# Performance work log

Hardware: AMD Instinct MI355X
Metric: run time of the kernel (lower is better)

Reference implementation:

```python
import jax, jax.numpy as jnp
import numpy as np

B, T, F, E, H = 8, 64, 16, 256, 8


def setup_inputs() -> dict:
    key = jax.random.key(0)
    ks = jax.random.split(key, 12)
    s = 1.0 / np.sqrt(E)
    return {
        "query": jax.random.normal(ks[0], (B, T, F, E), dtype=jnp.float32),
        "key": jax.random.normal(ks[1], (B, T, F, E), dtype=jnp.float32),
        "value": jax.random.normal(ks[2], (B, T, F, E), dtype=jnp.float32),
        "Wq": jax.random.uniform(ks[3], (E, E), jnp.float32, -s, s),
        "bq": jax.random.uniform(ks[4], (E,), jnp.float32, -s, s),
        "Wk": jax.random.uniform(ks[5], (E, E), jnp.float32, -s, s),
        "bk": jax.random.uniform(ks[6], (E,), jnp.float32, -s, s),
        "Wv": jax.random.uniform(ks[7], (E, E), jnp.float32, -s, s),
        "bv": jax.random.uniform(ks[8], (E,), jnp.float32, -s, s),
        "Wo": jax.random.uniform(ks[9], (E, E), jnp.float32, -s, s),
        "bo": jax.random.uniform(ks[10], (E,), jnp.float32, -s, s),
        "num_heads": H,
    }


def reference(query, key, value, Wq, bq, Wk, bk, Wv, bv, Wo, bo, num_heads):
    b, t, f, e = query.shape
    h = num_heads
    d = e // h

    def split_heads(x):
        # (b,t,f,e) -> (b,h,t,f,d)
        return x.reshape(b, t, f, h, d).transpose(0, 3, 1, 2, 4)

    q = split_heads(query @ Wq + bq)
    k = split_heads(key @ Wk + bk)
    v = split_heads(value @ Wv + bv)

    # scores[b,h,t,f,x,y] = k[b,h,t,f]·q[b,h,x,y] / sqrt(d)
    scores = jnp.einsum('bhtfd,bhxyd->bhtfxy', k, q) / jnp.sqrt(jnp.asarray(d, q.dtype))
    # Softmax2d on (b*h, t*f, t, f): softmax over channel = key positions (t*f)
    scores = scores.reshape(b, h, t * f, t, f)
    w = jax.nn.softmax(scores, axis=2)
    # out einsum 'bhtfxy,bhtfd->bhtfd': value scaled by total weight over queries
    s = w.sum(axis=(3, 4)).reshape(b, h, t, f)  # (b,h,t,f)
    out = v * s[..., None]
    out = out.transpose(0, 2, 3, 1, 4).reshape(b, t, f, e)
    return out @ Wo + bo
```

## Files before the change

### kernel.cpp

```cpp
#include <hip/hip_runtime.h>
#include <hip/hip_bf16.h>
#include <cstdint>
#include <cstddef>

constexpr int E = 256;
constexpr int H = 8;
constexpr int D = 32;
constexpr int N = 1024;
constexpr int R = 8192;
constexpr int BH = 64;
constexpr float SCALE = 0.17677669529663687f;
constexpr float LOG2E = 1.4426950408889634f;
constexpr float QSCALE = SCALE * LOG2E;


typedef __attribute__((ext_vector_type(8))) short short8;
typedef __attribute__((ext_vector_type(4))) short short4v;
typedef __attribute__((ext_vector_type(4))) float f32x4;

static __device__ __forceinline__ short bf16bits(float x) {
    __hip_bfloat16 h = __float2bfloat16(x);
    return *reinterpret_cast<short*>(&h);
}
static __device__ __forceinline__ float bf16tof(short s) {
    unsigned int u = ((unsigned int)(unsigned short)s) << 16;
    return *reinterpret_cast<float*>(&u);
}

__global__ __launch_bounds__(256) void convw_kernel(
    const float* __restrict__ Wq, const float* __restrict__ Wk,
    const float* __restrict__ Wv, const float* __restrict__ Wo,
    short* __restrict__ Wt4f)
{
    const int w = blockIdx.y;
    const float* src = (w == 0) ? Wq : (w == 1) ? Wk : (w == 2) ? Wv : Wo;
    const int tr = blockIdx.x >> 2, tc = blockIdx.x & 3;
    __shared__ float tile[64][65];
    const int tid = threadIdx.x;
    #pragma unroll
    for (int it = 0; it < 16; ++it) {
        int idx = tid + it * 256;
        int r = idx >> 6, c = idx & 63;
        tile[r][c] = src[(size_t)(tr * 64 + r) * E + tc * 64 + c];
    }
    __syncthreads();
    #pragma unroll
    for (int it = 0; it < 16; ++it) {
        int idx = tid + it * 256;
        int kk = idx >> 6, nn = idx & 63;
        int k = tr * 64 + kk, n = tc * 64 + nn;
        size_t didx = ((((size_t)w * 16 + (n >> 4)) * 32 + (k >> 3)) * 16 + (n & 15)) * 8 + (k & 7);
        Wt4f[didx] = bf16bits(tile[kk][nn]);
    }
}

__global__ __launch_bounds__(256) void proj_mfma(
    const float* __restrict__ q_in, const float* __restrict__ k_in, const float* __restrict__ v_in,
    const short* __restrict__ Wt4f,
    const float* __restrict__ bq, const float* __restrict__ bk, const float* __restrict__ bv,
    short* __restrict__ Qf, short* __restrict__ Kf,
    short* __restrict__ Vf, float* __restrict__ sfull)
{
    const int gid   = blockIdx.x;
    const int low3  = gid & 7;
    const int nhalf = (gid >> 3) & 1;
    const int p     = (gid >> 4) * 8 + low3;
    const int which = p >> 7;
    const int mblk  = p & 127;

    const float* X  = (which == 0) ? q_in : (which == 1) ? k_in : v_in;
    const float* bias = (which == 0) ? bq : (which == 1) ? bk : bv;

    if (which == 2) {
        int zb = mblk * 2 + nhalf;
        sfull[(size_t)zb * 256 + threadIdx.x] = 0.f;
    }

    const int wave = threadIdx.x >> 6, lane = threadIdx.x & 63;
    const int l15 = lane & 15, lhi = lane >> 4;
    const int m0 = mblk * 64 + wave * 16;
    const int n0 = nhalf * 128;

    __shared__ short Dt[4][16][16];

    const float* xrow = X + (size_t)(m0 + l15) * E + lhi * 8;

    f32x4 acc[8] = {};
    for (int k0 = 0; k0 < E; k0 += 32) {
        float4 a0 = *(const float4*)(xrow + k0);
        float4 a1 = *(const float4*)(xrow + k0 + 4);
        short at[8];
        at[0] = bf16bits(a0.x); at[1] = bf16bits(a0.y);
        at[2] = bf16bits(a0.z); at[3] = bf16bits(a0.w);
        at[4] = bf16bits(a1.x); at[5] = bf16bits(a1.y);
        at[6] = bf16bits(a1.z); at[7] = bf16bits(a1.w);
        short8 af = *(short8*)at;
        #pragma unroll
        for (int nt = 0; nt < 8; ++nt) {
            size_t bidx = ((((size_t)which * 16 + (n0 >> 4) + nt) * 32 + (k0 >> 3) + lhi) * 16 + l15) * 8;
            short8 bf = *(const short8*)(Wt4f + bidx);
            acc[nt] = __builtin_amdgcn_mfma_f32_16x16x32_bf16(af, bf, acc[nt], 0, 0, 0);
        }
    }

    short* dst;
    const int L = lane;
    #pragma unroll
    for (int nt = 0; nt < 8; ++nt) {
        const int ncol = n0 + nt * 16;
        #pragma unroll
        for (int j = 0; j < 4; ++j) {
            float v = acc[nt][j] + bias[ncol + l15];
            short sv = (which == 0) ? bf16bits(v * QSCALE) : bf16bits(v);
            Dt[wave][lhi * 4 + j][l15] = sv;
        }
        short4v rv = *(const short4v*)&Dt[wave][(L >> 1) & 15][(L >> 5) * 8 + (L & 1) * 4];

        size_t off;
        if (which == 2) {
            int tile = m0 >> 4;
            int kc0  = ncol >> 3;
            off = ((size_t)tile * 32 + kc0) * 128;
            dst = Vf;
        } else {
            int b = m0 >> 10, nl0 = m0 & (N - 1);
            int h = ncol >> 5, dd0 = ncol & 31;
            int tile = (b * H + h) * 64 + (nl0 >> 4);
            off = ((size_t)tile * 4 + (dd0 >> 3)) * 128;
            dst = (which == 0) ? Qf : Kf;
        }
        *(short4v*)(dst + off + (size_t)L * 4) = rv;
    }
}

__global__ __launch_bounds__(512, 4) void scores_fused(
    const short* __restrict__ Qf, const short* __restrict__ Kf,
    float* __restrict__ sfull)
{
    const int bh = blockIdx.x;
    const int mc = blockIdx.y;
    const int tid  = threadIdx.x;
    const int wave = tid >> 6;
    const int lane = tid & 63;
    const int l15  = lane & 15;
    const int lhi  = lane >> 4;

    const short* Qb = Qf + (size_t)bh * 32768;
    const short* Kb = Kf + (size_t)bh * 32768;

    __shared__ float zred[8][16];
    __shared__ float cinvS[16];

    short8 qf = *(const short8*)(Qb + ((size_t)mc * 4 + lhi) * 128 + l15 * 8);

    float z[4] = {0.f, 0.f, 0.f, 0.f};
    short4v ep[8];

    #pragma unroll
    for (int ntl = 0; ntl < 8; ++ntl) {
        int nt = wave * 8 + ntl;
        short8 kf = *(const short8*)(Kb + ((size_t)nt * 4 + lhi) * 128 + l15 * 8);
        f32x4 acc = {0.f, 0.f, 0.f, 0.f};
        acc = __builtin_amdgcn_mfma_f32_16x16x32_bf16(qf, kf, acc, 0, 0, 0);
        float e0 = exp2f(acc[0]), e1 = exp2f(acc[1]);
        float e2 = exp2f(acc[2]), e3 = exp2f(acc[3]);
        z[0] += e0; z[1] += e1; z[2] += e2; z[3] += e3;
        short4v pk = { bf16bits(e0), bf16bits(e1), bf16bits(e2), bf16bits(e3) };
        ep[ntl] = pk;
    }

    #pragma unroll
    for (int j = 0; j < 4; ++j) {
        float v = z[j];
        v += __shfl_xor(v, 1); v += __shfl_xor(v, 2);
        v += __shfl_xor(v, 4); v += __shfl_xor(v, 8);
        z[j] = v;
    }
    if (l15 == 0) {
        #pragma unroll
        for (int j = 0; j < 4; ++j)
            zred[wave][lhi * 4 + j] = z[j];
    }
    __syncthreads();
    if (tid < 16) {
        float zs = 0.f;
        #pragma unroll
        for (int w = 0; w < 8; ++w) zs += zred[w][tid];
        cinvS[tid] = 1.0f / zs;
    }
    __syncthreads();

    float ci[4];
    #pragma unroll
    for (int j = 0; j < 4; ++j) ci[j] = cinvS[lhi * 4 + j];

    float* sf = sfull + (size_t)bh * N;
    #pragma unroll
    for (int ntl = 0; ntl < 8; ++ntl) {
        int nt = wave * 8 + ntl;
        float rp = bf16tof(ep[ntl][0]) * ci[0] + bf16tof(ep[ntl][1]) * ci[1]
                 + bf16tof(ep[ntl][2]) * ci[2] + bf16tof(ep[ntl][3]) * ci[3];
        rp += __shfl_xor(rp, 16);
        rp += __shfl_xor(rp, 32);
        if (lane < 16) atomicAdd(&sf[nt * 16 + l15], rp);
    }
}

__global__ __launch_bounds__(256) void out_mfma(
    const short* __restrict__ Vf, const float* __restrict__ sfull,
    const short* __restrict__ Wt4f,
    const float* __restrict__ bo, float* __restrict__ out)
{
    const int gid  = blockIdx.x;
    const int low3 = gid & 7;
    const int nb   = (gid >> 3) & 3;
    const int q    = (gid >> 5) * 8 + low3;

    const int wave = threadIdx.x >> 6, lane = threadIdx.x & 63;
    const int l15 = lane & 15, lhi = lane >> 4;
    const int m0 = q * 64 + wave * 16;
    const int n0 = nb * 64;

    const int r = m0 + l15;
    const int b = r >> 10, nl = r & (N - 1);
    float sarr[8];
    #pragma unroll
    for (int h = 0; h < 8; ++h)
        sarr[h] = sfull[(size_t)(b * H + h) * N + nl];

    const short* vt = Vf + (size_t)(m0 >> 4) * 4096;

    f32x4 acc[4] = {};
    for (int k0 = 0; k0 < E; k0 += 32) {
        const float s = sarr[k0 >> 5];
        short8 vv = *(const short8*)(vt + ((size_t)(k0 >> 3) + lhi) * 128 + l15 * 8);
        short at[8];
        #pragma unroll
        for (int i = 0; i < 8; ++i) at[i] = bf16bits(bf16tof(vv[i]) * s);
        short8 af = *(short8*)at;
        #pragma unroll
        for (int nt = 0; nt < 4; ++nt) {
            size_t bidx = ((((size_t)3 * 16 + (n0 >> 4) + nt) * 32 + (k0 >> 3) + lhi) * 16 + l15) * 8;
            short8 bf = *(const short8*)(Wt4f + bidx);
            acc[nt] = __builtin_amdgcn_mfma_f32_16x16x32_bf16(af, bf, acc[nt], 0, 0, 0);
        }
    }
    #pragma unroll
    for (int nt = 0; nt < 4; ++nt) {
        #pragma unroll
        for (int j = 0; j < 4; ++j) {
            int m = m0 + lhi * 4 + j;
            int n = n0 + nt * 16 + l15;
            out[(size_t)m * E + n] = acc[nt][j] + bo[n];
        }
    }
}

extern "C" void kernel_launch(void* const* d_in, const int* in_sizes, int n_in,
                              void* d_out, int out_size, void* d_ws, size_t ws_size,
                              hipStream_t stream) {
    const float* q_in = (const float*)d_in[0];
    const float* k_in = (const float*)d_in[1];
    const float* v_in = (const float*)d_in[2];
    const float* Wq = (const float*)d_in[3];
    const float* bq = (const float*)d_in[4];
    const float* Wk = (const float*)d_in[5];
    const float* bk = (const float*)d_in[6];
    const float* Wv = (const float*)d_in[7];
    const float* bv = (const float*)d_in[8];
    const float* Wo = (const float*)d_in[9];
    const float* bo = (const float*)d_in[10];
    float* out = (float*)d_out;

    char* ws = (char*)d_ws;
    short* Wt4f  = (short*)ws;
    short* Qf    = (short*)(ws + (512u << 10));
    short* Kf    = (short*)(ws + (4u << 20) + (512u << 10));
    short* Vf    = (short*)(ws + (8u << 20) + (512u << 10));
    float* sfull = (float*)(ws + (12u << 20) + (512u << 10));

    convw_kernel<<<dim3(16, 4), 256, 0, stream>>>(Wq, Wk, Wv, Wo, Wt4f);

    proj_mfma<<<768, 256, 0, stream>>>(
        q_in, k_in, v_in, Wt4f, bq, bk, bv, Qf, Kf, Vf, sfull);

    scores_fused<<<dim3(BH, 64), 512, 0, stream>>>(Qf, Kf, sfull);

    out_mfma<<<512, 256, 0, stream>>>(Vf, sfull, Wt4f, bo, out);
}
```

Measured before the change: 61.47 us.

## Fuse weight bf16 conversion into projection kernels via shared-memory staging

Removes the separate weight-conversion kernel launch. Each projection and output block now reads its fp32 weight slice from global memory, converts it to bf16, and stages it in shared memory in MFMA fragment layout. The MFMA B operands are then read from LDS instead of a pre-converted global buffer. This saves one launch and its dependency, but every block repeats the weight conversion, and the proj kernel adds extra barriers and a second staging phase.

After: 85.50 us. 39.1% more time.

```diff
diff --git a/kernel.cpp b/kernel.cpp
--- a/kernel.cpp
+++ b/kernel.cpp
@@ -27,36 +27,9 @@
     return *reinterpret_cast<float*>(&u);
 }
 
-__global__ __launch_bounds__(256) void convw_kernel(
-    const float* __restrict__ Wq, const float* __restrict__ Wk,
-    const float* __restrict__ Wv, const float* __restrict__ Wo,
-    short* __restrict__ Wt4f)
-{
-    const int w = blockIdx.y;
-    const float* src = (w == 0) ? Wq : (w == 1) ? Wk : (w == 2) ? Wv : Wo;
-    const int tr = blockIdx.x >> 2, tc = blockIdx.x & 3;
-    __shared__ float tile[64][65];
-    const int tid = threadIdx.x;
-    #pragma unroll
-    for (int it = 0; it < 16; ++it) {
-        int idx = tid + it * 256;
-        int r = idx >> 6, c = idx & 63;
-        tile[r][c] = src[(size_t)(tr * 64 + r) * E + tc * 64 + c];
-    }
-    __syncthreads();
-    #pragma unroll
-    for (int it = 0; it < 16; ++it) {
-        int idx = tid + it * 256;
-        int kk = idx >> 6, nn = idx & 63;
-        int k = tr * 64 + kk, n = tc * 64 + nn;
-        size_t didx = ((((size_t)w * 16 + (n >> 4)) * 32 + (k >> 3)) * 16 + (n & 15)) * 8 + (k & 7);
-        Wt4f[didx] = bf16bits(tile[kk][nn]);
-    }
-}
-
 __global__ __launch_bounds__(256) void proj_mfma(
     const float* __restrict__ q_in, const float* __restrict__ k_in, const float* __restrict__ v_in,
-    const short* __restrict__ Wt4f,
+    const float* __restrict__ Wq, const float* __restrict__ Wk, const float* __restrict__ Wv,
     const float* __restrict__ bq, const float* __restrict__ bk, const float* __restrict__ bv,
     short* __restrict__ Qf, short* __restrict__ Kf,
     short* __restrict__ Vf, float* __restrict__ sfull)
@@ -69,6 +42,7 @@
     const int mblk  = p & 127;
 
     const float* X  = (which == 0) ? q_in : (which == 1) ? k_in : v_in;
+    const float* W  = (which == 0) ? Wq : (which == 1) ? Wk : Wv;
     const float* bias = (which == 0) ? bq : (which == 1) ? bk : bv;
 
     if (which == 2) {
@@ -76,30 +50,50 @@
         sfull[(size_t)zb * 256 + threadIdx.x] = 0.f;
     }
 
-    const int wave = threadIdx.x >> 6, lane = threadIdx.x & 63;
+    const int tid  = threadIdx.x;
+    const int wave = tid >> 6, lane = tid & 63;
     const int l15 = lane & 15, lhi = lane >> 4;
     const int m0 = mblk * 64 + wave * 16;
     const int n0 = nhalf * 128;
 
+    __shared__ short Wl[4 * 32 * 16 * 8];
     __shared__ short Dt[4][16][16];
 
     const float* xrow = X + (size_t)(m0 + l15) * E + lhi * 8;
 
     f32x4 acc[8] = {};
-    for (int k0 = 0; k0 < E; k0 += 32) {
-        float4 a0 = *(const float4*)(xrow + k0);
-        float4 a1 = *(const float4*)(xrow + k0 + 4);
-        short at[8];
-        at[0] = bf16bits(a0.x); at[1] = bf16bits(a0.y);
-        at[2] = bf16bits(a0.z); at[3] = bf16bits(a0.w);
-        at[4] = bf16bits(a1.x); at[5] = bf16bits(a1.y);
-        at[6] = bf16bits(a1.z); at[7] = bf16bits(a1.w);
-        short8 af = *(short8*)at;
-        #pragma unroll
-        for (int nt = 0; nt < 8; ++nt) {
-            size_t bidx = ((((size_t)which * 16 + (n0 >> 4) + nt) * 32 + (k0 >> 3) + lhi) * 16 + l15) * 8;
-            short8 bf = *(const short8*)(Wt4f + bidx);
-            acc[nt] = __builtin_amdgcn_mfma_f32_16x16x32_bf16(af, bf, acc[nt], 0, 0, 0);
+    #pragma unroll
+    for (int ph = 0; ph < 2; ++ph) {
+        __syncthreads();
+        #pragma unroll
+        for (int it = 0; it < 16; ++it) {
+            int k   = it * 16 + (tid >> 4);
+            int nlq = (tid & 15) * 4;
+            float4 w4 = *(const float4*)(W + (size_t)k * E + n0 + ph * 64 + nlq);
+            #pragma unroll
+            for (int e = 0; e < 4; ++e) {
+                int nl = nlq + e;
+                int idx = (((nl >> 4) * 32 + (k >> 3)) * 16 + (nl & 15)) * 8 + (k & 7);
+                Wl[idx] = bf16bits(e == 0 ? w4.x : e == 1 ? w4.y : e == 2 ? w4.z : w4.w);
+            }
+        }
+        __syncthreads();
+
+        for (int k0 = 0; k0 < E; k0 += 32) {
+            float4 a0 = *(const float4*)(xrow + k0);
+            float4 a1 = *(const float4*)(xrow + k0 + 4);
+            short at[8];
+            at[0] = bf16bits(a0.x); at[1] = bf16bits(a0.y);
+            at[2] = bf16bits(a0.z); at[3] = bf16bits(a0.w);
+            at[4] = bf16bits(a1.x); at[5] = bf16bits(a1.y);
+            at[6] = bf16bits(a1.z); at[7] = bf16bits(a1.w);
+            short8 af = *(short8*)at;
+            #pragma unroll
+            for (int ntl = 0; ntl < 4; ++ntl) {
+                int bidx = ((ntl * 32 + (k0 >> 3) + lhi) * 16 + l15) * 8;
+                short8 bf = *(const short8*)(Wl + bidx);
+                acc[ph * 4 + ntl] = __builtin_amdgcn_mfma_f32_16x16x32_bf16(af, bf, acc[ph * 4 + ntl], 0, 0, 0);
+            }
         }
     }
 
@@ -124,9 +118,9 @@
             dst = Vf;
         } else {
             int b = m0 >> 10, nl0 = m0 & (N - 1);
-            int h = ncol >> 5, dd0 = ncol & 31;
+            int h = ncol >> 5;
             int tile = (b * H + h) * 64 + (nl0 >> 4);
-            off = ((size_t)tile * 4 + (dd0 >> 3)) * 128;
+            off = ((size_t)tile * 4 + ((ncol & 31) >> 3)) * 128;
             dst = (which == 0) ? Qf : Kf;
         }
         *(short4v*)(dst + off + (size_t)L * 4) = rv;
@@ -208,7 +202,7 @@
 
 __global__ __launch_bounds__(256) void out_mfma(
     const short* __restrict__ Vf, const float* __restrict__ sfull,
-    const short* __restrict__ Wt4f,
+    const float* __restrict__ Wo,
     const float* __restrict__ bo, float* __restrict__ out)
 {
     const int gid  = blockIdx.x;
@@ -216,17 +210,35 @@
     const int nb   = (gid >> 3) & 3;
     const int q    = (gid >> 5) * 8 + low3;
 
-    const int wave = threadIdx.x >> 6, lane = threadIdx.x & 63;
+    const int tid  = threadIdx.x;
+    const int wave = tid >> 6, lane = tid & 63;
     const int l15 = lane & 15, lhi = lane >> 4;
     const int m0 = q * 64 + wave * 16;
     const int n0 = nb * 64;
 
+    __shared__ short Wl[4 * 32 * 16 * 8];
+
+    #pragma unroll
+    for (int it = 0; it < 16; ++it) {
+        int k   = it * 16 + (tid >> 4);
+        int nlq = (tid & 15) * 4;
+        float4 w4 = *(const float4*)(Wo + (size_t)k * E + n0 + nlq);
+        #pragma unroll
+        for (int e = 0; e < 4; ++e) {
+            int nl = nlq + e;
+            int idx = (((nl >> 4) * 32 + (k >> 3)) * 16 + (nl & 15)) * 8 + (k & 7);
+            Wl[idx] = bf16bits(e == 0 ? w4.x : e == 1 ? w4.y : e == 2 ? w4.z : w4.w);
+        }
+    }
+
     const int r = m0 + l15;
     const int b = r >> 10, nl = r & (N - 1);
     float sarr[8];
     #pragma unroll
     for (int h = 0; h < 8; ++h)
         sarr[h] = sfull[(size_t)(b * H + h) * N + nl];
+
+    __syncthreads();
 
     const short* vt = Vf + (size_t)(m0 >> 4) * 4096;
 
@@ -239,10 +251,10 @@
         for (int i = 0; i < 8; ++i) at[i] = bf16bits(bf16tof(vv[i]) * s);
         short8 af = *(short8*)at;
         #pragma unroll
-        for (int nt = 0; nt < 4; ++nt) {
-            size_t bidx = ((((size_t)3 * 16 + (n0 >> 4) + nt) * 32 + (k0 >> 3) + lhi) * 16 + l15) * 8;
-            short8 bf = *(const short8*)(Wt4f + bidx);
-            acc[nt] = __builtin_amdgcn_mfma_f32_16x16x32_bf16(af, bf, acc[nt], 0, 0, 0);
+        for (int ntl = 0; ntl < 4; ++ntl) {
+            int bidx = ((ntl * 32 + (k0 >> 3) + lhi) * 16 + l15) * 8;
+            short8 bf = *(const short8*)(Wl + bidx);
+            acc[ntl] = __builtin_amdgcn_mfma_f32_16x16x32_bf16(af, bf, acc[ntl], 0, 0, 0);
         }
     }
     #pragma unroll
@@ -273,18 +285,15 @@
     float* out = (float*)d_out;
 
     char* ws = (char*)d_ws;
-    short* Wt4f  = (short*)ws;
-    short* Qf    = (short*)(ws + (512u << 10));
-    short* Kf    = (short*)(ws + (4u << 20) + (512u << 10));
-    short* Vf    = (short*)(ws + (8u << 20) + (512u << 10));
-    float* sfull = (float*)(ws + (12u << 20) + (512u << 10));
-
-    convw_kernel<<<dim3(16, 4), 256, 0, stream>>>(Wq, Wk, Wv, Wo, Wt4f);
+    short* Qf    = (short*)ws;
+    short* Kf    = (short*)(ws + (4u << 20));
+    short* Vf    = (short*)(ws + (8u << 20));
+    float* sfull = (float*)(ws + (12u << 20));
 
     proj_mfma<<<768, 256, 0, stream>>>(
-        q_in, k_in, v_in, Wt4f, bq, bk, bv, Qf, Kf, Vf, sfull);
+        q_in, k_in, v_in, Wq, Wk, Wv, bq, bk, bv, Qf, Kf, Vf, sfull);
 
     scores_fused<<<dim3(BH, 64), 512, 0, stream>>>(Qf, Kf, sfull);
 
-    out_mfma<<<512, 256, 0, stream>>>(Vf, sfull, Wt4f, bo, out);
-}
+    out_mfma<<<512, 256, 0, stream>>>(Vf, sfull, Wo, bo, out);
+}
```
